# Kernel optimization log

Hardware: AMD Instinct MI355X
Metric: run time of the kernel (lower is better)

The kernel has to match this reference:

```python
import jax, jax.numpy as jnp
import numpy as np

DX = 0.01  # grid spacing for both x and z finite-difference kernels
SLOPE = 0.1
EPS = 1e-5


def fd_x(u):
    # central difference along last (x) axis, zero padding: (u[j+1]-u[j-1]) * 0.5/dx
    up = jnp.pad(u, ((0, 0), (0, 0), (0, 0), (1, 1)))
    return (up[..., 2:] - up[..., :-2]) * (0.5 / DX)


def fd_z(u):
    # central difference along z axis, zero padding: (u[i+1]-u[i-1]) * 0.5/dz
    up = jnp.pad(u, ((0, 0), (0, 0), (1, 1), (0, 0)))
    return (up[..., 2:, :] - up[..., :-2, :]) * (0.5 / DX)


def spectral_conv(x, w):
    # x: [B, Ci, NS, NZ, NX]; w: [4, Ci, Co, m1, m2, m3, 2]
    B, C, NS, NZ, NX = x.shape
    m1, m2, m3 = w.shape[3], w.shape[4], w.shape[5]
    xf = jnp.fft.fftn(x, axes=(-3, -2, -1), norm='forward')
    wc = w[..., 0] + 1j * w[..., 1]
    mul = lambda a, b: jnp.einsum('bixyz,ioxyz->boxyz', a, b)
    out = jnp.zeros((B, w.shape[2], NS, NZ, NX // 2 + 1), dtype=xf.dtype)
    out = out.at[:, :, :m1, :m2, :m3].set(mul(xf[:, :, :m1, :m2, :m3], wc[0]))
    out = out.at[:, :, -m1:, :m2, :m3].set(mul(xf[:, :, -m1:, :m2, :m3], wc[1]))
    out = out.at[:, :, :m1, -m2:, :m3].set(mul(xf[:, :, :m1, -m2:, :m3], wc[2]))
    out = out.at[:, :, -m1:, -m2:, :m3].set(mul(xf[:, :, -m1:, -m2:, :m3], wc[3]))
    # ifftn zero-pads last axis from NX//2+1 back to NX (matches torch semantics)
    return jnp.fft.ifftn(out, s=(NS, NZ, NX), axes=(-3, -2, -1), norm='forward').real


def batchnorm(x, g, b):
    # training-mode BatchNorm3d over (B, ns, z, x) per channel, biased variance
    m = x.mean(axis=(0, 2, 3, 4), keepdims=True)
    v = x.var(axis=(0, 2, 3, 4), keepdims=True)
    return (x - m) * jax.lax.rsqrt(v + EPS) * g[None, :, None, None, None] + b[None, :, None, None, None]


def setup_inputs() -> dict:
    key = jax.random.key(0)
    B, NS, NZ, NX = 2, 32, 96, 96
    C = 32
    M1, M2, M3 = 8, 12, 12
    ks = jax.random.split(key, 20)
    scale = 1.0 / (C * C)
    f32 = jnp.float32
    inp = {
        'x': jax.random.normal(ks[0], (B, NS, NZ, NX, 2), f32),
        'y': jax.random.uniform(ks[1], (B, NS, NZ, NX), f32),
        'fc0_w': jax.random.normal(ks[2], (2, C), f32) * 0.5,
        'fc0_b': jnp.zeros((C,), f32),
        'spec_w': jax.random.uniform(ks[3], (4, 4, C, C, M1, M2, M3, 2), f32) * scale,
        'w_w': jax.random.normal(ks[4], (4, C, C), f32) * (1.0 / np.sqrt(C)),
        'w_b': jnp.zeros((4, C), f32),
        'bn_g': jnp.ones((4, C), f32),
        'bn_b': jnp.zeros((4, C), f32),
        'fc1_w': jax.random.normal(ks[5], (C, 128), f32) * (1.0 / np.sqrt(C)),
        'fc1_b': jnp.zeros((128,), f32),
        'fc2_w': jax.random.normal(ks[6], (128, 64), f32) * (1.0 / np.sqrt(128)),
        'fc2_b': jnp.zeros((64,), f32),
        'fc3_w': jax.random.normal(ks[7], (64, 32), f32) * (1.0 / np.sqrt(64)),
        'fc3_b': jnp.zeros((32,), f32),
        'fc4_w': jax.random.normal(ks[8], (32, 64), f32) * (1.0 / np.sqrt(32)),
        'fc4_b': jnp.zeros((64,), f32),
        'fc5_w': jax.random.normal(ks[9], (64, 128), f32) * (1.0 / np.sqrt(64)),
        'fc5_b': jnp.zeros((128,), f32),
        'fc7_w': jax.random.normal(ks[10], (128, 1), f32) * (1.0 / np.sqrt(128)),
        'fc7_b': jnp.zeros((1,), f32),
    }
    return inp


def reference(x, y, fc0_w, fc0_b, spec_w, w_w, w_b, bn_g, bn_b,
              fc1_w, fc1_b, fc2_w, fc2_b, fc3_w, fc3_b, fc4_w, fc4_b,
              fc5_w, fc5_b, fc7_w, fc7_b):
    T0 = x[..., 1]                              # [B, ns, z, x]
    T0_dx = fd_x(T0)
    T0_dz = fd_z(T0)

    h = x @ fc0_w + fc0_b                       # [B, ns, z, x, C]
    h = jnp.transpose(h, (0, 4, 1, 2, 3))       # [B, C, ns, z, x]
    for i in range(4):
        h1 = spectral_conv(h, spec_w[i])
        h2 = jnp.einsum('oi,binzx->bonzx', w_w[i], h) + w_b[i][None, :, None, None, None]
        h = jax.nn.leaky_relu(batchnorm(h1 + h2, bn_g[i], bn_b[i]), SLOPE)
    h = jnp.transpose(h, (0, 2, 3, 4, 1))       # [B, ns, z, x, C]

    act = lambda u: jax.nn.leaky_relu(u, SLOPE)
    h = act(h @ fc1_w + fc1_b)
    h = act(h @ fc2_w + fc2_b)
    h = act(h @ fc3_w + fc3_b)
    h = act(h @ fc4_w + fc4_b)
    h = act(h @ fc5_w + fc5_b)
    tau = (h @ fc7_w + fc7_b)[..., 0]           # [B, ns, z, x]

    mask = jnp.where(T0 < 0.01, T0, jnp.ones_like(T0))
    mask = mask.at[:, :, 0:2, :].set(0.0)
    tau = tau * mask

    tau_dx = fd_x(tau)
    tau_dz = fd_z(tau)
    loss = (tau_dx + T0_dx) ** 2 + (tau_dz + T0_dz) ** 2 - y
    return (tau, loss)
```

## Files before the change

kernel.cpp:

```cpp
#include <hip/hip_runtime.h>
#include <math.h>

constexpr int B_ = 2, C_ = 32, NS = 32, NZ = 96, NX = 96;
constexpr int KS = 16, KZ = 24, KX = 12;
constexpr int NPTS = B_ * NS * NZ * NX;
constexpr int CHS  = NS * NZ * NX;
constexpr size_t HSIZE = (size_t)B_ * C_ * CHS;

constexpr size_t FX_C  = (size_t)B_ * C_ * NS * KX * NZ;
constexpr size_t FZX_C = (size_t)B_ * C_ * KZ * KX * NS;
constexpr size_t FS_C  = (size_t)B_ * C_ * KS * KZ * KX;

constexpr size_t OFF_HA   = 0;
constexpr size_t OFF_HB   = OFF_HA + HSIZE;
constexpr size_t OFF_FX   = OFF_HB + HSIZE;
constexpr size_t OFF_FZX  = OFF_FX + 2 * FX_C;
constexpr size_t OFF_FS   = OFF_FZX + 2 * FZX_C;
constexpr size_t OFF_G    = OFF_FS + 2 * FS_C;
constexpr size_t OFF_ST   = OFF_G + 2 * FS_C;
constexpr size_t OFF_SC   = OFF_ST + 256;
constexpr size_t OFF_TWXF = OFF_SC + 256;
constexpr size_t OFF_TWZF = OFF_TWXF + 2 * 96 * 12;
constexpr size_t OFF_TWSF = OFF_TWZF + 2 * 96 * 24;
constexpr size_t OFF_TWSI = OFF_TWSF + 2 * 32 * 16;
constexpr size_t OFF_TWZI = OFF_TWSI + 2 * 16 * 32;
constexpr size_t OFF_TWXI = OFF_TWZI + 2 * 24 * 96;

__global__ void k_init_tw(float* ws) {
  const double TWO_PI = 6.283185307179586476925286766559;
  int t = threadIdx.x;
  float2* twxf = (float2*)(ws + OFF_TWXF);
  for (int i = t; i < 96 * 12; i += 256) {
    int x = i / 12, k = i % 12;
    double a = -TWO_PI * (double)((k * x) % 96) / 96.0;
    twxf[i] = make_float2((float)cos(a), (float)sin(a));
  }
  float2* twzf = (float2*)(ws + OFF_TWZF);
  for (int i = t; i < 96 * 24; i += 256) {
    int z = i / 24, k = i % 24;
    double a = -TWO_PI * (double)((k * z) % 96) / 96.0;
    twzf[i] = make_float2((float)cos(a), (float)sin(a));
  }
  float2* twsf = (float2*)(ws + OFF_TWSF);
  const double SC = 1.0 / (double)(NS * NZ * NX);
  for (int i = t; i < 32 * 16; i += 256) {
    int s = i / 16, k = i % 16;
    int f = (k < 8) ? k : k + 16;
    double a = -TWO_PI * (double)((f * s) % 32) / 32.0;
    twsf[i] = make_float2((float)(cos(a) * SC), (float)(sin(a) * SC));
  }
  float2* twsi = (float2*)(ws + OFF_TWSI);
  for (int i = t; i < 16 * 32; i += 256) {
    int k = i / 32, s = i % 32;
    int f = (k < 8) ? k : k + 16;
    double a = TWO_PI * (double)((f * s) % 32) / 32.0;
    twsi[i] = make_float2((float)cos(a), (float)sin(a));
  }
  float2* twzi = (float2*)(ws + OFF_TWZI);
  for (int i = t; i < 24 * 96; i += 256) {
    int k = i / 96, z = i % 96;
    int f = (k < 12) ? k : k + 72;
    double a = TWO_PI * (double)((f * z) % 96) / 96.0;
    twzi[i] = make_float2((float)cos(a), (float)sin(a));
  }
  float2* twxi = (float2*)(ws + OFF_TWXI);
  for (int i = t; i < 12 * 96; i += 256) {
    int k = i / 96, x = i % 96;
    double a = TWO_PI * (double)((k * x) % 96) / 96.0;
    twxi[i] = make_float2((float)cos(a), (float)sin(a));
  }
}

__global__ void k_zero_stats(float* st) {
  st[threadIdx.x] = 0.f;
}

__global__ void k_fc0(const float* __restrict__ xin, const float* __restrict__ w,
                      const float* __restrict__ bias, float* __restrict__ h) {
  int pt = blockIdx.x * 256 + threadIdx.x;
  float2 xv = ((const float2*)xin)[pt];
  size_t base = (size_t)(pt / CHS) * C_ * CHS + (pt % CHS);
  for (int c = 0; c < C_; ++c)
    h[base + (size_t)c * CHS] = xv.x * w[c] + xv.y * w[C_ + c] + bias[c];
}

__global__ __launch_bounds__(256) void k_fwd(const float* __restrict__ h, float2* __restrict__ fzx,
                      const float2* __restrict__ twxf, const float2* __restrict__ twzf,
                      const float* __restrict__ sc, int use_bn) {
  __shared__ float  sh_h[96 * 97];
  __shared__ float2 sh_fx[96 * 12];
  int t = threadIdx.x;
  int bcs = blockIdx.x;
  int s = bcs & 31;
  int bc = bcs >> 5;
  int c = bc & 31;
  float scale = use_bn ? sc[c] : 1.f;
  float shift = use_bn ? sc[32 + c] : 0.f;
  float lk = use_bn ? 0.1f : 1.0f;
  const float* hp = h + (size_t)bc * CHS + (size_t)s * (NZ * NX);
  for (int i = t; i < NZ * NX; i += 256) {
    float v = hp[i];
    v = v * scale + shift;
    v = v >= 0.f ? v : v * lk;
    sh_h[(i / 96) * 97 + (i % 96)] = v;
  }
  __syncthreads();
  {
    int half = __builtin_amdgcn_readfirstlane(t >> 7);
    int z = t & 127;
    if (z < 96) {
      float ar[6], ai[6];
      #pragma unroll
      for (int j = 0; j < 6; ++j) { ar[j] = 0.f; ai[j] = 0.f; }
      const float2* twx = twxf + half * 6;
      const float* row = sh_h + z * 97;
      for (int x = 0; x < 96; ++x) {
        float v = row[x];
        #pragma unroll
        for (int j = 0; j < 6; ++j) {
          float2 w = twx[x * 12 + j];
          ar[j] += v * w.x; ai[j] += v * w.y;
        }
      }
      #pragma unroll
      for (int j = 0; j < 6; ++j)
        sh_fx[z * 12 + half * 6 + j] = make_float2(ar[j], ai[j]);
    }
  }
  __syncthreads();
  float2* outp = fzx + (size_t)bcs * 288;
  for (int it = t; it < 288; it += 256) {
    int kx = it % 12, kz = it / 12;
    float ar0 = 0.f, ai0 = 0.f, ar1 = 0.f, ai1 = 0.f;
    for (int z = 0; z < 96; z += 2) {
      float2 v0 = sh_fx[z * 12 + kx];
      float2 w0 = twzf[z * 24 + kz];
      float2 v1 = sh_fx[(z + 1) * 12 + kx];
      float2 w1 = twzf[(z + 1) * 24 + kz];
      ar0 += v0.x * w0.x - v0.y * w0.y;
      ai0 += v0.x * w0.y + v0.y * w0.x;
      ar1 += v1.x * w1.x - v1.y * w1.y;
      ai1 += v1.x * w1.y + v1.y * w1.x;
    }
    outp[it] = make_float2(ar0 + ar1, ai0 + ai1);
  }
}

__global__ __launch_bounds__(256) void k_dfts(const float2* __restrict__ fzx, float2* __restrict__ fs,
                       const float2* __restrict__ tw) {
  int tid = blockIdx.x * 256 + threadIdx.x;
  int kzkx = tid % 288;
  int ks = (tid / 288) & 15;
  int bc = tid / 4608;
  const float2* src = fzx + (size_t)bc * (32 * 288) + kzkx;
  float ar = 0.f, ai = 0.f;
  #pragma unroll 8
  for (int s = 0; s < 32; ++s) {
    float2 v = src[s * 288];
    float2 w = tw[s * 16 + ks];
    ar += v.x * w.x - v.y * w.y;
    ai += v.x * w.y + v.y * w.x;
  }
  fs[(size_t)bc * 4608 + ks * 288 + kzkx] = make_float2(ar, ai);
}

__global__ __launch_bounds__(256) void k_mix(const float2* __restrict__ fs, const float* __restrict__ spec,
                      int l, float2* __restrict__ g) {
  int tid = blockIdx.x * 256 + threadIdx.x;
  int m = tid % 1152;
  int o = (tid / 1152) & 31;
  int q = tid / 36864;
  int m1 = m / 144, r = m - m1 * 144, m2 = r / 12, m3 = r - m2 * 12;
  int ks = m1 + (q & 1) * 8;
  int kz = m2 + ((q >> 1) & 1) * 12;
  int fidx = (ks * KZ + kz) * KX + m3;
  const float2* w2 = (const float2*)spec;
  size_t widx = ((size_t)(l * 4 + q) * 1024 + o) * 1152 + m;
  const float2* f0 = fs + fidx;
  const float2* f1 = fs + (size_t)C_ * 4608 + fidx;
  float a0r = 0.f, a0i = 0.f, a1r = 0.f, a1i = 0.f;
  #pragma unroll 4
  for (int i = 0; i < C_; ++i) {
    float2 w = w2[widx];  widx += 36864;
    float2 v0 = f0[(size_t)i * 4608];
    float2 v1 = f1[(size_t)i * 4608];
    a0r += v0.x * w.x - v0.y * w.y;  a0i += v0.x * w.y + v0.y * w.x;
    a1r += v1.x * w.x - v1.y * w.y;  a1i += v1.x * w.y + v1.y * w.x;
  }
  g[(size_t)o * 4608 + fidx] = make_float2(a0r, a0i);
  g[(size_t)(C_ + o) * 4608 + fidx] = make_float2(a1r, a1i);
}

__global__ __launch_bounds__(256) void k_idfts(const float2* __restrict__ g, float2* __restrict__ gs,
                        const float2* __restrict__ tw) {
  int tid = blockIdx.x * 256 + threadIdx.x;
  int kzkx = tid % 288;
  int s = (tid / 288) & 31;
  int bo = tid / 9216;
  const float2* src = g + (size_t)bo * 4608 + kzkx;
  float ar = 0.f, ai = 0.f;
  #pragma unroll
  for (int ks = 0; ks < 16; ++ks) {
    float2 v = src[ks * 288];
    float2 w = tw[ks * 32 + s];
    ar += v.x * w.x - v.y * w.y;
    ai += v.x * w.y + v.y * w.x;
  }
  gs[((size_t)bo * 32 + s) * 288 + kzkx] = make_float2(ar, ai);
}

__global__ __launch_bounds__(256) void k_idftz(const float2* __restrict__ gs, float2* __restrict__ gz,
                        const float2* __restrict__ tw) {
  int tid = blockIdx.x * 256 + threadIdx.x;
  int kx = tid % 12;
  int z = (tid / 12) % 96;
  int s = (tid / 1152) & 31;
  int bo = tid / 36864;
  const float2* src = gs + ((size_t)bo * 32 + s) * 288 + kx;
  float ar = 0.f, ai = 0.f;
  #pragma unroll 8
  for (int kz = 0; kz < 24; ++kz) {
    float2 v = src[kz * 12];
    float2 w = tw[kz * 96 + z];
    ar += v.x * w.x - v.y * w.y;
    ai += v.x * w.y + v.y * w.x;
  }
  gz[(((size_t)bo * 32 + s) * 96 + z) * 12 + kx] = make_float2(ar, ai);
}

__global__ __launch_bounds__(256) void k_idftx_fuse(const float2* __restrict__ gz, const float* __restrict__ hsrc,
                             const float* __restrict__ ww, const float* __restrict__ wb,
                             const float2* __restrict__ twxi, const float* __restrict__ sc,
                             int use_bn, float* __restrict__ adst) {
  __shared__ float  sh_h[C_ * NX];
  __shared__ float2 sh_g[C_ * KX];
  int blk = blockIdx.x;
  int z = blk % NZ, s = (blk / NZ) % NS, b = blk / (NZ * NS);
  int t = threadIdx.x;
  size_t rowbase = ((size_t)b * C_) * CHS + (size_t)s * (NZ * NX) + (size_t)z * NX;
  float lk = use_bn ? 0.1f : 1.0f;
  for (int i = t; i < C_ * NX; i += 256) {
    int c = i / NX, x = i % NX;
    float v = hsrc[rowbase + (size_t)c * CHS + x];
    float scl = use_bn ? sc[c] : 1.f;
    float shf = use_bn ? sc[32 + c] : 0.f;
    v = v * scl + shf;
    sh_h[i] = v >= 0.f ? v : v * lk;
  }
  for (int i = t; i < C_ * KX; i += 256) {
    int o = i / KX, kx = i % KX;
    sh_g[i] = gz[(((size_t)(b * C_ + o) * NS + s) * NZ + z) * KX + kx];
  }
  __syncthreads();
  int x = t & 127;
  int og = __builtin_amdgcn_readfirstlane(t >> 7);
  if (x >= NX) return;
  float2 tw[KX];
  #pragma unroll
  for (int k = 0; k < KX; ++k) tw[k] = twxi[k * NX + x];
  float acc[16];
  #pragma unroll
  for (int j = 0; j < 16; ++j) {
    int o = og * 16 + j;
    float a = wb[o];
    const float2* gp = sh_g + o * KX;
    #pragma unroll
    for (int k = 0; k < KX; ++k) {
      float2 gv = gp[k];
      a += gv.x * tw[k].x - gv.y * tw[k].y;
    }
    acc[j] = a;
  }
  for (int i = 0; i < C_; ++i) {
    float val = sh_h[i * NX + x];
    #pragma unroll
    for (int j = 0; j < 16; ++j) acc[j] += ww[(og * 16 + j) * C_ + i] * val;
  }
  #pragma unroll
  for (int j = 0; j < 16; ++j)
    adst[rowbase + (size_t)(og * 16 + j) * CHS + x] = acc[j];
}

__global__ void k_bnstats(const float* __restrict__ a, float* __restrict__ st) {
  int bc = blockIdx.x >> 4;
  int chunk = blockIdx.x & 15;
  const float4* p = (const float4*)(a + (size_t)bc * CHS + (size_t)chunk * 18432);
  float s = 0.f, s2 = 0.f;
  for (int i = threadIdx.x; i < 4608; i += 256) {
    float4 v = p[i];
    s += v.x + v.y + v.z + v.w;
    s2 += v.x * v.x + v.y * v.y + v.z * v.z + v.w * v.w;
  }
  for (int off = 32; off > 0; off >>= 1) {
    s  += __shfl_down(s, off);
    s2 += __shfl_down(s2, off);
  }
  __shared__ float rs[4], rs2[4];
  if ((threadIdx.x & 63) == 0) { rs[threadIdx.x >> 6] = s; rs2[threadIdx.x >> 6] = s2; }
  __syncthreads();
  if (threadIdx.x == 0) {
    float S = rs[0] + rs[1] + rs[2] + rs[3];
    float S2 = rs2[0] + rs2[1] + rs2[2] + rs2[3];
    int c = bc & 31;
    atomicAdd(&st[c], S);
    atomicAdd(&st[32 + c], S2);
  }
}

__global__ void k_bnfinal(const float* __restrict__ st, const float* __restrict__ g,
                          const float* __restrict__ bb, float* __restrict__ sc) {
  int c = threadIdx.x;
  if (c >= 32) return;
  const float N = (float)NPTS;
  float mean = st[c] / N;
  float var = st[32 + c] / N - mean * mean;
  float inv = rsqrtf(var + 1e-5f);
  float scale = inv * g[c];
  sc[c] = scale;
  sc[32 + c] = bb[c] - mean * scale;
}

__global__ __launch_bounds__(512, 6) void k_mlp(
    const float* __restrict__ h, const float* __restrict__ xin,
    const float* __restrict__ sc,
    const float* __restrict__ w1, const float* __restrict__ b1,
    const float* __restrict__ w2, const float* __restrict__ b2,
    const float* __restrict__ w3, const float* __restrict__ b3,
    const float* __restrict__ w4, const float* __restrict__ b4,
    const float* __restrict__ w5, const float* __restrict__ b5,
    const float* __restrict__ w7, const float* __restrict__ b7,
    float* __restrict__ out) {
  __shared__ float A[64 * 65];
  __shared__ float Bf[64 * 129];
  __shared__ float P[64 * 9];
  int t = threadIdx.x;
  int p = t & 63;
  int q = __builtin_amdgcn_readfirstlane(t >> 6);
  int pt0 = blockIdx.x * 64;

  for (int i = t; i < 64 * 32; i += 512) {
    int c = i >> 6, pp = i & 63;
    int pt = pt0 + pp;
    size_t base = (size_t)(pt / CHS) * C_ * CHS + (pt % CHS);
    float v = h[base + (size_t)c * CHS];
    v = v * sc[c] + sc[32 + c];
    A[pp * 65 + c] = v >= 0.f ? v : 0.1f * v;
  }
  __syncthreads();

  {
    const int m0 = q * 16;
    float acc[16];
    #pragma unroll
    for (int j = 0; j < 16; ++j) acc[j] = b1[m0 + j];
    const float* arow = A + p * 65;
    #pragma unroll 4
    for (int k = 0; k < 32; ++k) {
      float a = arow[k];
      const float* wr = w1 + k * 128 + m0;
      #pragma unroll
      for (int j = 0; j < 16; ++j) acc[j] += a * wr[j];
    }
    float* brow = Bf + p * 129 + m0;
    #pragma unroll
    for (int j = 0; j < 16; ++j) {
      float v = acc[j];
      brow[j] = v >= 0.f ? v : 0.1f * v;
    }
  }
  __syncthreads();

  {
    const int m0 = q * 8;
    float acc[8];
    #pragma unroll
    for (int j = 0; j < 8; ++j) acc[j] = b2[m0 + j];
    const float* brow = Bf + p * 129;
    #pragma unroll 4
    for (int k = 0; k < 128; ++k) {
      float a = brow[k];
      const float* wr = w2 + k * 64 + m0;
      #pragma unroll
      for (int j = 0; j < 8; ++j) acc[j] += a * wr[j];
    }
    float* arow = A + p * 65 + m0;
    #pragma unroll
    for (int j = 0; j < 8; ++j) {
      float v = acc[j];
      arow[j] = v >= 0.f ? v : 0.1f * v;
    }
  }
  __syncthreads();

  {
    const int m0 = q * 4;
    float acc[4];
    #pragma unroll
    for (int j = 0; j < 4; ++j) acc[j] = b3[m0 + j];
    const float* arow = A + p * 65;
    #pragma unroll 4
    for (int k = 0; k < 64; ++k) {
      float a = arow[k];
      const float* wr = w3 + k * 32 + m0;
      #pragma unroll
      for (int j = 0; j < 4; ++j) acc[j] += a * wr[j];
    }
    float* brow = Bf + p * 129 + m0;
    #pragma unroll
    for (int j = 0; j < 4; ++j) {
      float v = acc[j];
      brow[j] = v >= 0.f ? v : 0.1f * v;
    }
  }
  __syncthreads();

  {
    const int m0 = q * 8;
    float acc[8];
    #pragma unroll
    for (int j = 0; j < 8; ++j) acc[j] = b4[m0 + j];
    const float* brow = Bf + p * 129;
    #pragma unroll 4
    for (int k = 0; k < 32; ++k) {
      float a = brow[k];
      const float* wr = w4 + k * 64 + m0;
      #pragma unroll
      for (int j = 0; j < 8; ++j) acc[j] += a * wr[j];
    }
    float* arow = A + p * 65 + m0;
    #pragma unroll
    for (int j = 0; j < 8; ++j) {
      float v = acc[j];
      arow[j] = v >= 0.f ? v : 0.1f * v;
    }
  }
  __syncthreads();

  {
    const int m0 = q * 16;
    float acc[16];
    #pragma unroll
    for (int j = 0; j < 16; ++j) acc[j] = b5[m0 + j];
    const float* arow = A + p * 65;
    #pragma unroll 4
    for (int k = 0; k < 64; ++k) {
      float a = arow[k];
      const float* wr = w5 + k * 128 + m0;
      #pragma unroll
      for (int j = 0; j < 16; ++j) acc[j] += a * wr[j];
    }
    float partial = 0.f;
    #pragma unroll
    for (int j = 0; j < 16; ++j) {
      float v = acc[j];
      v = v >= 0.f ? v : 0.1f * v;
      partial += v * w7[m0 + j];
    }
    P[p * 9 + q] = partial;
  }
  __syncthreads();

  if (q == 0) {
    int pt = pt0 + p;
    float acc = b7[0];
    #pragma unroll
    for (int j = 0; j < 8; ++j) acc += P[p * 9 + j];
    float T0 = xin[2 * pt + 1];
    float mask = (T0 < 0.01f) ? T0 : 1.0f;
    int z = (pt / NX) % NZ;
    if (z < 2) mask = 0.f;
    out[pt] = acc * mask;
  }
}

__global__ void k_loss(const float* __restrict__ tau, const float* __restrict__ xin,
                       const float* __restrict__ y, float* __restrict__ loss) {
  int pt = blockIdx.x * 256 + threadIdx.x;
  int x = pt % NX, z = (pt / NX) % NZ;
  float tpx = (x < NX - 1) ? tau[pt + 1] : 0.f;
  float tmx = (x > 0) ? tau[pt - 1] : 0.f;
  float tpz = (z < NZ - 1) ? tau[pt + NX] : 0.f;
  float tmz = (z > 0) ? tau[pt - NX] : 0.f;
  float Tpx = (x < NX - 1) ? xin[2 * (pt + 1) + 1] : 0.f;
  float Tmx = (x > 0) ? xin[2 * (pt - 1) + 1] : 0.f;
  float Tpz = (z < NZ - 1) ? xin[2 * (pt + NX) + 1] : 0.f;
  float Tmz = (z > 0) ? xin[2 * (pt - NX) + 1] : 0.f;
  float dx = (tpx - tmx) * 50.f + (Tpx - Tmx) * 50.f;
  float dz = (tpz - tmz) * 50.f + (Tpz - Tmz) * 50.f;
  loss[pt] = dx * dx + dz * dz - y[pt];
}

extern "C" void kernel_launch(void* const* d_in, const int* in_sizes, int n_in,
                              void* d_out, int out_size, void* d_ws, size_t ws_size,
                              hipStream_t stream) {
  (void)in_sizes; (void)n_in; (void)out_size; (void)ws_size;
  const float* xin    = (const float*)d_in[0];
  const float* y      = (const float*)d_in[1];
  const float* fc0_w  = (const float*)d_in[2];
  const float* fc0_b  = (const float*)d_in[3];
  const float* spec_w = (const float*)d_in[4];
  const float* w_w    = (const float*)d_in[5];
  const float* w_b    = (const float*)d_in[6];
  const float* bn_g   = (const float*)d_in[7];
  const float* bn_b   = (const float*)d_in[8];
  const float* fc1_w  = (const float*)d_in[9];
  const float* fc1_b  = (const float*)d_in[10];
  const float* fc2_w  = (const float*)d_in[11];
  const float* fc2_b  = (const float*)d_in[12];
  const float* fc3_w  = (const float*)d_in[13];
  const float* fc3_b  = (const float*)d_in[14];
  const float* fc4_w  = (const float*)d_in[15];
  const float* fc4_b  = (const float*)d_in[16];
  const float* fc5_w  = (const float*)d_in[17];
  const float* fc5_b  = (const float*)d_in[18];
  const float* fc7_w  = (const float*)d_in[19];
  const float* fc7_b  = (const float*)d_in[20];
  float* ws  = (float*)d_ws;
  float* out = (float*)d_out;

  k_init_tw<<<1, 256, 0, stream>>>(ws);
  k_zero_stats<<<1, 256, 0, stream>>>(ws + OFF_ST);
  k_fc0<<<NPTS / 256, 256, 0, stream>>>(xin, fc0_w, fc0_b, ws + OFF_HA);

  float* hsrc = ws + OFF_HA;
  float* hdst = ws + OFF_HB;
  for (int l = 0; l < 4; ++l) {
    const float* sc_prev = ws + OFF_SC + (size_t)(l - 1) * 64;
    int use_bn = (l > 0) ? 1 : 0;
    k_fwd<<<B_ * C_ * NS, 256, 0, stream>>>(hsrc, (float2*)(ws + OFF_FZX),
                                            (const float2*)(ws + OFF_TWXF),
                                            (const float2*)(ws + OFF_TWZF), sc_prev, use_bn);
    k_dfts<<<1152, 256, 0, stream>>>((const float2*)(ws + OFF_FZX), (float2*)(ws + OFF_FS),
                                     (const float2*)(ws + OFF_TWSF));
    k_mix<<<576, 256, 0, stream>>>((const float2*)(ws + OFF_FS), spec_w, l,
                                   (float2*)(ws + OFF_G));
    k_idfts<<<2304, 256, 0, stream>>>((const float2*)(ws + OFF_G), (float2*)(ws + OFF_FZX),
                                      (const float2*)(ws + OFF_TWSI));
    k_idftz<<<9216, 256, 0, stream>>>((const float2*)(ws + OFF_FZX), (float2*)(ws + OFF_FX),
                                      (const float2*)(ws + OFF_TWZI));
    k_idftx_fuse<<<B_ * NS * NZ, 256, 0, stream>>>((const float2*)(ws + OFF_FX), hsrc,
                                                   w_w + (size_t)l * C_ * C_, w_b + (size_t)l * C_,
                                                   (const float2*)(ws + OFF_TWXI), sc_prev,
                                                   use_bn, hdst);
    k_bnstats<<<1024, 256, 0, stream>>>(hdst, ws + OFF_ST + (size_t)l * 64);
    k_bnfinal<<<1, 64, 0, stream>>>(ws + OFF_ST + (size_t)l * 64, bn_g + (size_t)l * C_,
                                    bn_b + (size_t)l * C_, ws + OFF_SC + (size_t)l * 64);
    float* tmp = hsrc; hsrc = hdst; hdst = tmp;
  }

  k_mlp<<<NPTS / 64, 512, 0, stream>>>(hsrc, xin, ws + OFF_SC + 192,
                                       fc1_w, fc1_b, fc2_w, fc2_b, fc3_w, fc3_b,
                                       fc4_w, fc4_b, fc5_w, fc5_b, fc7_w, fc7_b, out);
  k_loss<<<NPTS / 256, 256, 0, stream>>>(out, xin, y, out + NPTS);
}
```

Measured before the change: 1.545 ms.

## Fuse inverse s/z DFTs, fold BN stats into idftx, split MLP launch

Merges the inverse DFT along s and z into one kernel. Each block stages a batch-channel spectrum slice in shared memory and computes the s-slice, then the z transform, without a global round trip. BatchNorm statistics are now accumulated inside k_idftx_fuse from the freshly computed outputs, which removes the separate k_bnstats pass over the full activation tensor but adds more atomics. The MLP launch is split into 8 sequential sub-launches with a block offset, which adds launch overhead for no clear benefit.

```diff
diff --git a/kernel.cpp b/kernel.cpp
--- a/kernel.cpp
+++ b/kernel.cpp
@@ -191,47 +191,47 @@
   g[(size_t)(C_ + o) * 4608 + fidx] = make_float2(a1r, a1i);
 }
 
-__global__ __launch_bounds__(256) void k_idfts(const float2* __restrict__ g, float2* __restrict__ gs,
-                        const float2* __restrict__ tw) {
-  int tid = blockIdx.x * 256 + threadIdx.x;
-  int kzkx = tid % 288;
-  int s = (tid / 288) & 31;
-  int bo = tid / 9216;
-  const float2* src = g + (size_t)bo * 4608 + kzkx;
-  float ar = 0.f, ai = 0.f;
-  #pragma unroll
-  for (int ks = 0; ks < 16; ++ks) {
-    float2 v = src[ks * 288];
-    float2 w = tw[ks * 32 + s];
-    ar += v.x * w.x - v.y * w.y;
-    ai += v.x * w.y + v.y * w.x;
-  }
-  gs[((size_t)bo * 32 + s) * 288 + kzkx] = make_float2(ar, ai);
-}
-
-__global__ __launch_bounds__(256) void k_idftz(const float2* __restrict__ gs, float2* __restrict__ gz,
-                        const float2* __restrict__ tw) {
-  int tid = blockIdx.x * 256 + threadIdx.x;
-  int kx = tid % 12;
-  int z = (tid / 12) % 96;
-  int s = (tid / 1152) & 31;
-  int bo = tid / 36864;
-  const float2* src = gs + ((size_t)bo * 32 + s) * 288 + kx;
-  float ar = 0.f, ai = 0.f;
-  #pragma unroll 8
-  for (int kz = 0; kz < 24; ++kz) {
-    float2 v = src[kz * 12];
-    float2 w = tw[kz * 96 + z];
-    ar += v.x * w.x - v.y * w.y;
-    ai += v.x * w.y + v.y * w.x;
-  }
-  gz[(((size_t)bo * 32 + s) * 96 + z) * 12 + kx] = make_float2(ar, ai);
+__global__ __launch_bounds__(256) void k_idft_sz(const float2* __restrict__ g, float2* __restrict__ gz,
+                        const float2* __restrict__ twsi, const float2* __restrict__ twzi) {
+  __shared__ float2 sh_g[4608];
+  __shared__ float2 sh_gs[288];
+  int t = threadIdx.x;
+  int bo = blockIdx.x >> 5;
+  int s  = blockIdx.x & 31;
+  const float2* gsrc = g + (size_t)bo * 4608;
+  for (int i = t; i < 4608; i += 256) sh_g[i] = gsrc[i];
+  __syncthreads();
+  for (int it = t; it < 288; it += 256) {
+    float ar = 0.f, ai = 0.f;
+    #pragma unroll
+    for (int ks = 0; ks < 16; ++ks) {
+      float2 v = sh_g[ks * 288 + it];
+      float2 w = twsi[ks * 32 + s];
+      ar += v.x * w.x - v.y * w.y;
+      ai += v.x * w.y + v.y * w.x;
+    }
+    sh_gs[it] = make_float2(ar, ai);
+  }
+  __syncthreads();
+  float2* outp = gz + (size_t)(bo * 32 + s) * 1152;
+  for (int it = t; it < 1152; it += 256) {
+    int kx = it % 12, z = it / 12;
+    float ar = 0.f, ai = 0.f;
+    #pragma unroll 8
+    for (int kz = 0; kz < 24; ++kz) {
+      float2 v = sh_gs[kz * 12 + kx];
+      float2 w = twzi[kz * 96 + z];
+      ar += v.x * w.x - v.y * w.y;
+      ai += v.x * w.y + v.y * w.x;
+    }
+    outp[it] = make_float2(ar, ai);
+  }
 }
 
 __global__ __launch_bounds__(256) void k_idftx_fuse(const float2* __restrict__ gz, const float* __restrict__ hsrc,
                              const float* __restrict__ ww, const float* __restrict__ wb,
                              const float2* __restrict__ twxi, const float* __restrict__ sc,
-                             int use_bn, float* __restrict__ adst) {
+                             int use_bn, float* __restrict__ adst, float* __restrict__ st) {
   __shared__ float  sh_h[C_ * NX];
   __shared__ float2 sh_g[C_ * KX];
   int blk = blockIdx.x;
@@ -254,56 +254,51 @@
   __syncthreads();
   int x = t & 127;
   int og = __builtin_amdgcn_readfirstlane(t >> 7);
-  if (x >= NX) return;
-  float2 tw[KX];
-  #pragma unroll
-  for (int k = 0; k < KX; ++k) tw[k] = twxi[k * NX + x];
   float acc[16];
-  #pragma unroll
-  for (int j = 0; j < 16; ++j) {
-    int o = og * 16 + j;
-    float a = wb[o];
-    const float2* gp = sh_g + o * KX;
-    #pragma unroll
-    for (int k = 0; k < KX; ++k) {
-      float2 gv = gp[k];
-      a += gv.x * tw[k].x - gv.y * tw[k].y;
-    }
-    acc[j] = a;
-  }
-  for (int i = 0; i < C_; ++i) {
-    float val = sh_h[i * NX + x];
-    #pragma unroll
-    for (int j = 0; j < 16; ++j) acc[j] += ww[(og * 16 + j) * C_ + i] * val;
-  }
-  #pragma unroll
-  for (int j = 0; j < 16; ++j)
-    adst[rowbase + (size_t)(og * 16 + j) * CHS + x] = acc[j];
-}
-
-__global__ void k_bnstats(const float* __restrict__ a, float* __restrict__ st) {
-  int bc = blockIdx.x >> 4;
-  int chunk = blockIdx.x & 15;
-  const float4* p = (const float4*)(a + (size_t)bc * CHS + (size_t)chunk * 18432);
-  float s = 0.f, s2 = 0.f;
-  for (int i = threadIdx.x; i < 4608; i += 256) {
-    float4 v = p[i];
-    s += v.x + v.y + v.z + v.w;
-    s2 += v.x * v.x + v.y * v.y + v.z * v.z + v.w * v.w;
-  }
-  for (int off = 32; off > 0; off >>= 1) {
-    s  += __shfl_down(s, off);
-    s2 += __shfl_down(s2, off);
-  }
-  __shared__ float rs[4], rs2[4];
-  if ((threadIdx.x & 63) == 0) { rs[threadIdx.x >> 6] = s; rs2[threadIdx.x >> 6] = s2; }
-  __syncthreads();
-  if (threadIdx.x == 0) {
-    float S = rs[0] + rs[1] + rs[2] + rs[3];
-    float S2 = rs2[0] + rs2[1] + rs2[2] + rs2[3];
-    int c = bc & 31;
-    atomicAdd(&st[c], S);
-    atomicAdd(&st[32 + c], S2);
+  if (x < NX) {
+    float2 tw[KX];
+    #pragma unroll
+    for (int k = 0; k < KX; ++k) tw[k] = twxi[k * NX + x];
+    #pragma unroll
+    for (int j = 0; j < 16; ++j) {
+      int o = og * 16 + j;
+      float a = wb[o];
+      const float2* gp = sh_g + o * KX;
+      #pragma unroll
+      for (int k = 0; k < KX; ++k) {
+        float2 gv = gp[k];
+        a += gv.x * tw[k].x - gv.y * tw[k].y;
+      }
+      acc[j] = a;
+    }
+    for (int i = 0; i < C_; ++i) {
+      float val = sh_h[i * NX + x];
+      #pragma unroll
+      for (int j = 0; j < 16; ++j) acc[j] += ww[(og * 16 + j) * C_ + i] * val;
+    }
+    #pragma unroll
+    for (int j = 0; j < 16; ++j)
+      adst[rowbase + (size_t)(og * 16 + j) * CHS + x] = acc[j];
+  }
+  __syncthreads();
+  if (x < NX) {
+    #pragma unroll
+    for (int j = 0; j < 16; ++j) sh_h[(og * 16 + j) * NX + x] = acc[j];
+  }
+  __syncthreads();
+  {
+    int o = t >> 3, ch = t & 7;
+    const float* row = sh_h + o * NX + ch * 12;
+    float s1 = 0.f, s2 = 0.f;
+    #pragma unroll
+    for (int k = 0; k < 12; ++k) { float v = row[k]; s1 += v; s2 += v * v; }
+    s1 += __shfl_down(s1, 4);  s2 += __shfl_down(s2, 4);
+    s1 += __shfl_down(s1, 2);  s2 += __shfl_down(s2, 2);
+    s1 += __shfl_down(s1, 1);  s2 += __shfl_down(s2, 1);
+    if (ch == 0) {
+      atomicAdd(&st[o], s1);
+      atomicAdd(&st[32 + o], s2);
+    }
   }
 }
 
@@ -322,7 +317,7 @@
 
 __global__ __launch_bounds__(512, 6) void k_mlp(
     const float* __restrict__ h, const float* __restrict__ xin,
-    const float* __restrict__ sc,
+    const float* __restrict__ sc, int blk0,
     const float* __restrict__ w1, const float* __restrict__ b1,
     const float* __restrict__ w2, const float* __restrict__ b2,
     const float* __restrict__ w3, const float* __restrict__ b3,
@@ -336,7 +331,7 @@
   int t = threadIdx.x;
   int p = t & 63;
   int q = __builtin_amdgcn_readfirstlane(t >> 6);
-  int pt0 = blockIdx.x * 64;
+  int pt0 = (blockIdx.x + blk0) * 64;
 
   for (int i = t; i < 64 * 32; i += 512) {
     int c = i >> 6, pp = i & 63;
@@ -534,22 +529,22 @@
                                      (const float2*)(ws + OFF_TWSF));
     k_mix<<<576, 256, 0, stream>>>((const float2*)(ws + OFF_FS), spec_w, l,
                                    (float2*)(ws + OFF_G));
-    k_idfts<<<2304, 256, 0, stream>>>((const float2*)(ws + OFF_G), (float2*)(ws + OFF_FZX),
-                                      (const float2*)(ws + OFF_TWSI));
-    k_idftz<<<9216, 256, 0, stream>>>((const float2*)(ws + OFF_FZX), (float2*)(ws + OFF_FX),
-                                      (const float2*)(ws + OFF_TWZI));
+    k_idft_sz<<<64 * 32, 256, 0, stream>>>((const float2*)(ws + OFF_G), (float2*)(ws + OFF_FX),
+                                           (const float2*)(ws + OFF_TWSI),
+                                           (const float2*)(ws + OFF_TWZI));
     k_idftx_fuse<<<B_ * NS * NZ, 256, 0, stream>>>((const float2*)(ws + OFF_FX), hsrc,
                                                    w_w + (size_t)l * C_ * C_, w_b + (size_t)l * C_,
                                                    (const float2*)(ws + OFF_TWXI), sc_prev,
-                                                   use_bn, hdst);
-    k_bnstats<<<1024, 256, 0, stream>>>(hdst, ws + OFF_ST + (size_t)l * 64);
+                                                   use_bn, hdst, ws + OFF_ST + (size_t)l * 64);
     k_bnfinal<<<1, 64, 0, stream>>>(ws + OFF_ST + (size_t)l * 64, bn_g + (size_t)l * C_,
                                     bn_b + (size_t)l * C_, ws + OFF_SC + (size_t)l * 64);
     float* tmp = hsrc; hsrc = hdst; hdst = tmp;
   }
 
-  k_mlp<<<NPTS / 64, 512, 0, stream>>>(hsrc, xin, ws + OFF_SC + 192,
-                                       fc1_w, fc1_b, fc2_w, fc2_b, fc3_w, fc3_b,
-                                       fc4_w, fc4_b, fc5_w, fc5_b, fc7_w, fc7_b, out);
+  for (int part = 0; part < 8; ++part) {
+    k_mlp<<<1152, 512, 0, stream>>>(hsrc, xin, ws + OFF_SC + 192, part * 1152,
+                                    fc1_w, fc1_b, fc2_w, fc2_b, fc3_w, fc3_b,
+                                    fc4_w, fc4_b, fc5_w, fc5_b, fc7_w, fc7_b, out);
+  }
   k_loss<<<NPTS / 256, 256, 0, stream>>>(out, xin, y, out + NPTS);
 }
```

After: 2.412 ms. +56.1%, slower.
